# Optimization experiments

Hardware: AMD Instinct MI355X
Metric: run time of the kernel (lower is better)

The kernel has to match this reference:

```python
import jax, jax.numpy as jnp
import numpy as np
from jax import lax

N = 2048
B = 8
CH = 10
START = 1
STOP = 65


def setup_inputs() -> dict:
    key = jax.random.key(0)
    ks = jax.random.split(key, 13)

    def g(k, s):
        return jax.random.normal(k, s, jnp.float32) * 0.05

    return {
        "x": jax.random.normal(ks[0], (B, 1, N, N), jnp.float32),
        "wl": g(ks[1], (CH // 2, 1, 3, N)), "bl": g(ks[2], (CH // 2,)),
        "wr": g(ks[3], (CH // 2, 1, N, 3)), "br": g(ks[4], (CH // 2,)),
        "wA": g(ks[5], (CH, CH, 3)), "bA": g(ks[6], (CH,)),
        "wB": g(ks[7], (CH, CH, 3)), "bB": g(ks[8], (CH,)),  # shared by layers 2&3 (torch list aliasing)
        "wT": g(ks[9], (CH, CH, 3)), "bT": g(ks[10], (CH,)),
        "wm": g(ks[11], (2, CH, 1)), "bm": g(ks[12], (2,)),
        "start": START, "stop": STOP,
    }


def _conv1d(h, w, b, pad):
    y = lax.conv_general_dilated(h, w, (1,), [(pad, pad)], dimension_numbers=("NCH", "OIH", "NCH"))
    return y + b[None, :, None]


def _forward(x, wl, bl, wr, br, wA, bA, wB, bB, wT, bT, wm, bm, start, stop):
    n = x.shape[-1]
    # scan_left: Conv2d kernel (3, n), padding (1, 0) -> (B, 5, n, 1) -> squeeze
    left_ = lax.conv_general_dilated(x, wl, (1, 1), [(1, 1), (0, 0)], dimension_numbers=("NCHW", "OIHW", "NCHW"))
    left_ = left_[..., 0] + bl[None, :, None]
    # scan_right: Conv2d kernel (n, 3), padding (0, 1) -> (B, 5, 1, n) -> squeeze
    right_ = lax.conv_general_dilated(x, wr, (1, 1), [(0, 0), (1, 1)], dimension_numbers=("NCHW", "OIHW", "NCHW"))
    right_ = right_[:, :, 0, :] + br[None, :, None]
    lr = jnp.concatenate([left_, right_], axis=1)  # (B, 10, n)
    h = jax.nn.relu(_conv1d(lr, wA, bA, 1))
    h = jax.nn.relu(_conv1d(h, wB, bB, 1))  # same weights twice: torch [conv, relu]*2 aliasing
    h = jax.nn.relu(_conv1d(h, wB, bB, 1))
    # ConvTranspose1d(k=3, stride=1, pad=1) == Conv1d with transposed, spatially-flipped kernel, pad=1
    wTc = jnp.flip(jnp.swapaxes(wT, 0, 1), -1)
    for _ in range(3):
        h = jax.nn.relu(_conv1d(h, wTc, bT, 1))
    m = jax.nn.sigmoid(_conv1d(h, wm, bm, 0))  # (B, 2, n)
    left, right = m[:, 0, :], m[:, 1, :]
    xs = x[:, 0]  # (B, n, n)
    preds = []
    for d in range(start, stop):  # static diagonal indices
        curr = jnp.exp(jnp.diagonal(xs, offset=d, axis1=1, axis2=2))  # (B, n-d)
        mass_in = curr[:, 1:] * right[:, 1:n - d] + curr[:, :-1] * left[:, d:n - 1]
        mass_out = right[:, 0:n - d - 1] + left[:, d + 1:n]
        p = jnp.log(mass_in / mass_out)
        preds.append(p - jnp.mean(p))  # scalar mean over batch+positions, as torch.mean
    return jnp.concatenate(preds, axis=1)  # ragged preds concatenated: (B, sum(n-d-1))


def reference(x, wl, bl, wr, br, wA, bA, wB, bB, wT, bT, wm, bm, start, stop):
    return _forward(x, wl, bl, wr, br, wA, bA, wB, bB, wT, bT, wm, bm, start, stop)
```

## Files before the change

kernel.cpp:

```cpp
#include <hip/hip_runtime.h>
#include <hip/hip_bf16.h>

#define NN 2048
#define BB 8
#define TROW 128928

typedef __attribute__((ext_vector_type(8))) short bf16x8;
typedef __attribute__((ext_vector_type(4))) float f32x4;

__device__ __forceinline__ short f2bf(float f) {
    unsigned u = __float_as_uint(f);
    unsigned r = (u + 0x7FFFu + ((u >> 16) & 1u)) >> 16;
    return (short)r;
}

__global__ __launch_bounds__(256) void k_stage1(const float* __restrict__ x,
                                                const float* __restrict__ wl,
                                                const float* __restrict__ wr,
                                                float* __restrict__ Rp,
                                                float* __restrict__ CSp,
                                                float* __restrict__ psum,
                                                int* __restrict__ counter) {
    int blk = blockIdx.x;
    int tid = threadIdx.x;
    if (blk == 0 && tid < 65) {
        if (tid < 64) psum[tid] = 0.f;
        else *counter = 0;
    }
    if (blk < 1024) {
        int b = blk >> 7;
        int sub = blk & 127;
        int rg = sub >> 2, ks = sub & 3;
        int wv = tid >> 6, lane = tid & 63;
        int q = lane >> 4, m = lane & 15;
        int r0 = rg * 64 + wv * 16;
        int nrow = (m == 15) ? 14 : m;
        int k0 = ks * 512 + q * 8;

        const float* ap = x + ((size_t)(b * NN + r0 + m)) * NN + k0;
        const float* bp = wl + (size_t)nrow * NN + k0;

        f32x4 acc = {0.f, 0.f, 0.f, 0.f};
#pragma unroll 4
        for (int it = 0; it < 16; it++) {
            const float* a0 = ap + it * 32;
            const float* b0 = bp + it * 32;
            float4 av0 = *(const float4*)(a0);
            float4 av1 = *(const float4*)(a0 + 4);
            float4 bv0 = *(const float4*)(b0);
            float4 bv1 = *(const float4*)(b0 + 4);
            bf16x8 af, bf;
            af[0] = f2bf(av0.x); af[1] = f2bf(av0.y); af[2] = f2bf(av0.z); af[3] = f2bf(av0.w);
            af[4] = f2bf(av1.x); af[5] = f2bf(av1.y); af[6] = f2bf(av1.z); af[7] = f2bf(av1.w);
            bf[0] = f2bf(bv0.x); bf[1] = f2bf(bv0.y); bf[2] = f2bf(bv0.z); bf[3] = f2bf(bv0.w);
            bf[4] = f2bf(bv1.x); bf[5] = f2bf(bv1.y); bf[6] = f2bf(bv1.z); bf[7] = f2bf(bv1.w);
            acc = __builtin_amdgcn_mfma_f32_16x16x32_bf16(af, bf, acc, 0, 0, 0);
        }
        float* rp = Rp + (size_t)ks * 262144 + ((size_t)b * NN + r0) * 16;
#pragma unroll
        for (int reg = 0; reg < 4; reg++)
            rp[(q * 4 + reg) * 16 + m] = acc[reg];
    } else {
        int blk2 = blk - 1024;
        int b = blk2 >> 5;
        int rem = blk2 & 31;
        int jc = rem >> 4, rc = rem & 15;
        int r0 = rc * 128;
        int c0 = jc * 1024 + tid * 4;
        const float* xp = x + ((size_t)b * NN + r0) * NN + c0;

        float acc[15][4];
#pragma unroll
        for (int k = 0; k < 15; k++)
#pragma unroll
            for (int e = 0; e < 4; e++) acc[k][e] = 0.f;

        for (int rb = 0; rb < 16; rb++) {
            float4 xv[8];
#pragma unroll
            for (int q = 0; q < 8; q++)
                xv[q] = *(const float4*)(xp + (size_t)(rb * 8 + q) * NN);
#pragma unroll
            for (int q = 0; q < 8; q++) {
                int h = r0 + rb * 8 + q;
#pragma unroll
                for (int k = 0; k < 15; k++) {
                    int c = k / 3, dw = k - c * 3;
                    float wk = wr[c * (NN * 3) + h * 3 + dw];
                    acc[k][0] = fmaf(xv[q].x, wk, acc[k][0]);
                    acc[k][1] = fmaf(xv[q].y, wk, acc[k][1]);
                    acc[k][2] = fmaf(xv[q].z, wk, acc[k][2]);
                    acc[k][3] = fmaf(xv[q].w, wk, acc[k][3]);
                }
            }
        }
        float* outp = CSp + ((size_t)(rc * BB + b) * 16) * NN + c0;
#pragma unroll
        for (int k = 0; k < 15; k++) {
            float4 v; v.x = acc[k][0]; v.y = acc[k][1]; v.z = acc[k][2]; v.w = acc[k][3];
            *(float4*)(outp + (size_t)k * NN) = v;
        }
    }
}

__global__ __launch_bounds__(256) void k_csum(const float* __restrict__ CSp,
                                              float* __restrict__ CS,
                                              const float* __restrict__ Rp,
                                              float* __restrict__ R) {
    int blk = blockIdx.x;
    if (blk < 256) {
        int vid = blk * 256 + threadIdx.x;
        const float4* src = (const float4*)CSp;
        float4 s = src[vid];
#pragma unroll
        for (int rc = 1; rc < 16; rc++) {
            float4 v = src[vid + rc * 65536];
            s.x += v.x; s.y += v.y; s.z += v.z; s.w += v.w;
        }
        ((float4*)CS)[vid] = s;
    } else {
        int vid = (blk - 256) * 256 + threadIdx.x;
        const float4* src = (const float4*)Rp;
        float4 s = src[vid];
#pragma unroll
        for (int ks = 1; ks < 4; ks++) {
            float4 v = src[vid + ks * 65536];
            s.x += v.x; s.y += v.y; s.z += v.z; s.w += v.w;
        }
        ((float4*)R)[vid] = s;
    }
}

__global__ __launch_bounds__(256) void k_chainC(const float* __restrict__ R,
                                                const float* __restrict__ CS,
                                                const float* __restrict__ bl,
                                                const float* __restrict__ br,
                                                const float* __restrict__ wA, const float* __restrict__ bA,
                                                const float* __restrict__ wB, const float* __restrict__ bB,
                                                const float* __restrict__ wT, const float* __restrict__ bT,
                                                const float* __restrict__ wm, const float* __restrict__ bm,
                                                float* __restrict__ LEFT, float* __restrict__ RIGHT) {
    __shared__ float buf0[10][144], buf1[10][144];
    __shared__ float W[3][10][10][3];
    __shared__ float Bs[3][10];
    __shared__ float Wm[2][10], Bm[2];
    int b = blockIdx.x >> 4;
    int c0 = (blockIdx.x & 15) << 7;
    int tid = threadIdx.x;

    for (int idx = tid; idx < 900; idx += 256) {
        int set = idx / 300, rem = idx - set * 300;
        int o = rem / 30, rem2 = rem - o * 30, c = rem2 / 3, kk = rem2 - c * 3;
        float u;
        if (set == 0) u = wA[o * 30 + c * 3 + kk];
        else if (set == 1) u = wB[o * 30 + c * 3 + kk];
        else u = wT[c * 30 + o * 3 + (2 - kk)];
        W[set][o][c][kk] = u;
    }
    if (tid < 30) {
        float v = (tid < 10) ? bA[tid] : (tid < 20) ? bB[tid - 10] : bT[tid - 20];
        Bs[tid / 10][tid % 10] = v;
    }
    if (tid < 20) Wm[tid / 10][tid % 10] = wm[tid];
    if (tid < 2) Bm[tid] = bm[tid];

    for (int idx = tid; idx < 1400; idx += 256) {
        int ch = idx / 140, p = idx - ch * 140;
        int g = c0 - 6 + p;
        float v = 0.f;
        if (g >= 0 && g < NN) {
            if (ch < 5) {
                v = bl[ch];
#pragma unroll
                for (int dh = 0; dh < 3; dh++) {
                    int r = g + dh - 1;
                    if (r >= 0 && r < NN) v += R[(size_t)(b * NN + r) * 16 + ch * 3 + dh];
                }
            } else {
                int c = ch - 5;
                v = br[c];
#pragma unroll
                for (int dw = 0; dw < 3; dw++) {
                    int j = g + dw - 1;
                    if (j >= 0 && j < NN)
                        v += CS[((size_t)b * 16 + c * 3 + dw) * NN + j];
                }
            }
        }
        buf0[ch][p] = v;
    }
    __syncthreads();

    float(*in)[144] = buf0;
    float(*out)[144] = buf1;
    for (int layer = 0; layer < 6; layer++) {
        int set = (layer == 0) ? 0 : (layer < 3 ? 1 : 2);
        int lo = layer + 1;
        for (int idx = tid; idx < 1400; idx += 256) {
            int o = idx / 140, p = idx - o * 140;
            if (p >= lo && p < 140 - lo) {
                float s = Bs[set][o];
#pragma unroll
                for (int c = 0; c < 10; c++) {
                    const float* ip = &in[c][p];
                    s = fmaf(ip[-1], W[set][o][c][0], s);
                    s = fmaf(ip[0], W[set][o][c][1], s);
                    s = fmaf(ip[1], W[set][o][c][2], s);
                }
                s = s > 0.f ? s : 0.f;
                int g = c0 - 6 + p;
                if (g < 0 || g >= NN) s = 0.f;
                out[o][p] = s;
            }
        }
        __syncthreads();
        float(*tmp)[144] = in; in = out; out = tmp;
    }
    {
        int idx = tid;
        int o = idx >> 7, pp = idx & 127;
        int p = 6 + pp;
        float s = Bm[o];
#pragma unroll
        for (int c = 0; c < 10; c++) s = fmaf(in[c][p], Wm[o][c], s);
        float sig = 1.f / (1.f + __expf(-s));
        (o ? RIGHT : LEFT)[b * NN + c0 + pp] = sig;
    }
}

__global__ __launch_bounds__(256) void k_diagout(const float* __restrict__ x,
                                                 const float* __restrict__ LEFT,
                                                 const float* __restrict__ RIGHT,
                                                 float* __restrict__ psum,
                                                 int* __restrict__ counter,
                                                 float* __restrict__ outp) {
    __shared__ float T[65][65];
    __shared__ float psl[64];
    int b = blockIdx.x >> 5;
    int i0 = (blockIdx.x & 31) << 6;
    int tid = threadIdx.x;

    for (int idx = tid; idx < 65 * 64; idx += 256) {
        int r = idx >> 6, dm1 = idx & 63;
        int row = i0 + r;
        int col = row + dm1 + 1;
        float v = 0.f;
        if (row < NN && col < NN) v = __expf(x[((size_t)b * NN + row) * NN + col]);
        T[r][dm1] = v;
    }
    __syncthreads();

    int wv = tid >> 6, lane = tid & 63;
    int i = i0 + lane;
    const float* lf = LEFT + b * NN;
    const float* rt = RIGHT + b * NN;
    float pv[16];
#pragma unroll
    for (int s = 0; s < 16; s++) {
        int dm1 = wv * 16 + s;
        int d = dm1 + 1;
        int L = (NN - 1) - d;
        float p = 0.f;
        if (i < L) {
            float mi = T[lane + 1][dm1] * rt[i + 1] + T[lane][dm1] * lf[d + i];
            float mo = rt[i] + lf[d + 1 + i];
            p = __logf(mi / mo);
        }
        pv[s] = p;
        float s64 = p;
        for (int off = 32; off; off >>= 1) s64 += __shfl_down(s64, off);
        if (lane == 0) psl[dm1] = s64;
    }
    __syncthreads();
    if (tid < 64) atomicAdd(&psum[tid], psl[tid]);
    __syncthreads();
    if (tid == 0) {
        __threadfence();
        atomicAdd(counter, 1);
        while (__hip_atomic_load(counter, __ATOMIC_ACQUIRE, __HIP_MEMORY_SCOPE_AGENT) < 256) {}
    }
    __syncthreads();
    if (tid < 64)
        psl[tid] = __hip_atomic_load(&psum[tid], __ATOMIC_RELAXED, __HIP_MEMORY_SCOPE_AGENT);
    __syncthreads();

#pragma unroll
    for (int s = 0; s < 16; s++) {
        int dm1 = wv * 16 + s;
        int d = dm1 + 1;
        int L = (NN - 1) - d;
        if (i < L) {
            float mean = psl[dm1] / (float)(8 * L);
            size_t off0 = (size_t)dm1 * (NN - 1) - (size_t)dm1 * (dm1 + 1) / 2;
            outp[(size_t)b * TROW + off0 + i] = pv[s] - mean;
        }
    }
}

extern "C" void kernel_launch(void* const* d_in, const int* in_sizes, int n_in,
                              void* d_out, int out_size, void* d_ws, size_t ws_size,
                              hipStream_t stream) {
    const float* x = (const float*)d_in[0];
    const float* wl = (const float*)d_in[1];
    const float* bl = (const float*)d_in[2];
    const float* wr = (const float*)d_in[3];
    const float* br = (const float*)d_in[4];
    const float* wA = (const float*)d_in[5];
    const float* bA = (const float*)d_in[6];
    const float* wB = (const float*)d_in[7];
    const float* bB = (const float*)d_in[8];
    const float* wT = (const float*)d_in[9];
    const float* bT = (const float*)d_in[10];
    const float* wm = (const float*)d_in[11];
    const float* bm = (const float*)d_in[12];

    float* ws = (float*)d_ws;
    float* R    = ws;
    float* Rp   = ws + 262144;
    float* CSp  = ws + 1310720;
    float* CS   = ws + 5505024;
    float* LEFT = ws + 5767168;
    float* RIGHT= ws + 5783552;
    float* psum = ws + 5799936;
    int*   counter = (int*)(ws + 5800000);

    k_stage1<<<1280, 256, 0, stream>>>(x, wl, wr, Rp, CSp, psum, counter);
    k_csum<<<512, 256, 0, stream>>>(CSp, CS, Rp, R);
    k_chainC<<<128, 256, 0, stream>>>(R, CS, bl, br, wA, bA, wB, bB, wT, bT, wm, bm, LEFT, RIGHT);
    k_diagout<<<256, 256, 0, stream>>>(x, LEFT, RIGHT, psum, counter, (float*)d_out);
}
```

Baseline: 294.6 us.

## Fuse reduction, conv chain and diagonal output into one kernel with grid barrier

Removes the split-K partial sums for the left scan, so each block runs the full K=2048 reduction and writes R directly. It drops the separate csum kernel by folding the 16-way column-partial reduction into the conv-chain stage. The conv chain and diagonal-output kernels are merged into one 256-block kernel that uses a software grid barrier to exchange LEFT/RIGHT, cutting two launches and some workspace traffic. The costs are fewer blocks in the MFMA stage (less parallelism, longer serial K loop), redundant halo recomputation per 64-wide tile, and a spin barrier that assumes all 256 blocks are co-resident.

```diff
diff --git a/kernel.cpp b/kernel.cpp
--- a/kernel.cpp
+++ b/kernel.cpp
@@ -1,5 +1,4 @@
 #include <hip/hip_runtime.h>
-#include <hip/hip_bf16.h>
 
 #define NN 2048
 #define BB 8
@@ -17,32 +16,30 @@
 __global__ __launch_bounds__(256) void k_stage1(const float* __restrict__ x,
                                                 const float* __restrict__ wl,
                                                 const float* __restrict__ wr,
-                                                float* __restrict__ Rp,
+                                                float* __restrict__ R,
                                                 float* __restrict__ CSp,
                                                 float* __restrict__ psum,
-                                                int* __restrict__ counter) {
+                                                int* __restrict__ counters) {
     int blk = blockIdx.x;
     int tid = threadIdx.x;
-    if (blk == 0 && tid < 65) {
+    if (blk == 0) {
         if (tid < 64) psum[tid] = 0.f;
-        else *counter = 0;
-    }
-    if (blk < 1024) {
-        int b = blk >> 7;
-        int sub = blk & 127;
-        int rg = sub >> 2, ks = sub & 3;
+        else if (tid < 66) counters[tid - 64] = 0;
+    }
+    if (blk < 256) {
+        int b = blk >> 5;
+        int rg = blk & 31;
         int wv = tid >> 6, lane = tid & 63;
         int q = lane >> 4, m = lane & 15;
         int r0 = rg * 64 + wv * 16;
         int nrow = (m == 15) ? 14 : m;
-        int k0 = ks * 512 + q * 8;
-
-        const float* ap = x + ((size_t)(b * NN + r0 + m)) * NN + k0;
-        const float* bp = wl + (size_t)nrow * NN + k0;
+
+        const float* ap = x + ((size_t)(b * NN + r0 + m)) * NN + q * 8;
+        const float* bp = wl + (size_t)nrow * NN + q * 8;
 
         f32x4 acc = {0.f, 0.f, 0.f, 0.f};
 #pragma unroll 4
-        for (int it = 0; it < 16; it++) {
+        for (int it = 0; it < 64; it++) {
             const float* a0 = ap + it * 32;
             const float* b0 = bp + it * 32;
             float4 av0 = *(const float4*)(a0);
@@ -56,12 +53,12 @@
             bf[4] = f2bf(bv1.x); bf[5] = f2bf(bv1.y); bf[6] = f2bf(bv1.z); bf[7] = f2bf(bv1.w);
             acc = __builtin_amdgcn_mfma_f32_16x16x32_bf16(af, bf, acc, 0, 0, 0);
         }
-        float* rp = Rp + (size_t)ks * 262144 + ((size_t)b * NN + r0) * 16;
+        float* rp = R + ((size_t)b * NN + r0) * 16;
 #pragma unroll
         for (int reg = 0; reg < 4; reg++)
             rp[(q * 4 + reg) * 16 + m] = acc[reg];
     } else {
-        int blk2 = blk - 1024;
+        int blk2 = blk - 256;
         int b = blk2 >> 5;
         int rem = blk2 & 31;
         int jc = rem >> 4, rc = rem & 15;
@@ -103,50 +100,41 @@
     }
 }
 
-__global__ __launch_bounds__(256) void k_csum(const float* __restrict__ CSp,
-                                              float* __restrict__ CS,
-                                              const float* __restrict__ Rp,
-                                              float* __restrict__ R) {
-    int blk = blockIdx.x;
-    if (blk < 256) {
-        int vid = blk * 256 + threadIdx.x;
-        const float4* src = (const float4*)CSp;
-        float4 s = src[vid];
-#pragma unroll
-        for (int rc = 1; rc < 16; rc++) {
-            float4 v = src[vid + rc * 65536];
-            s.x += v.x; s.y += v.y; s.z += v.z; s.w += v.w;
-        }
-        ((float4*)CS)[vid] = s;
-    } else {
-        int vid = (blk - 256) * 256 + threadIdx.x;
-        const float4* src = (const float4*)Rp;
-        float4 s = src[vid];
-#pragma unroll
-        for (int ks = 1; ks < 4; ks++) {
-            float4 v = src[vid + ks * 65536];
-            s.x += v.x; s.y += v.y; s.z += v.z; s.w += v.w;
-        }
-        ((float4*)R)[vid] = s;
-    }
-}
-
-__global__ __launch_bounds__(256) void k_chainC(const float* __restrict__ R,
-                                                const float* __restrict__ CS,
-                                                const float* __restrict__ bl,
-                                                const float* __restrict__ br,
-                                                const float* __restrict__ wA, const float* __restrict__ bA,
-                                                const float* __restrict__ wB, const float* __restrict__ bB,
-                                                const float* __restrict__ wT, const float* __restrict__ bT,
-                                                const float* __restrict__ wm, const float* __restrict__ bm,
-                                                float* __restrict__ LEFT, float* __restrict__ RIGHT) {
-    __shared__ float buf0[10][144], buf1[10][144];
+__global__ __launch_bounds__(256) void k_rest(const float* __restrict__ x,
+                                              const float* __restrict__ R,
+                                              const float* __restrict__ CSp,
+                                              const float* __restrict__ bl,
+                                              const float* __restrict__ br,
+                                              const float* __restrict__ wA, const float* __restrict__ bA,
+                                              const float* __restrict__ wB, const float* __restrict__ bB,
+                                              const float* __restrict__ wT, const float* __restrict__ bT,
+                                              const float* __restrict__ wm, const float* __restrict__ bm,
+                                              float* __restrict__ LEFT, float* __restrict__ RIGHT,
+                                              float* __restrict__ psum,
+                                              int* __restrict__ counters,
+                                              float* __restrict__ outp) {
+    __shared__ float T[65][65];
+    __shared__ float buf0[10][80], buf1[10][80];
     __shared__ float W[3][10][10][3];
     __shared__ float Bs[3][10];
     __shared__ float Wm[2][10], Bm[2];
-    int b = blockIdx.x >> 4;
-    int c0 = (blockIdx.x & 15) << 7;
+    __shared__ float psl[64];
+    __shared__ float lfs[132], rts[68];
+
+    int b = blockIdx.x >> 5;
+    int t5 = blockIdx.x & 31;
+    int c0 = t5 << 6;
+    int i0 = t5 << 6;
     int tid = threadIdx.x;
+
+    for (int idx = tid; idx < 65 * 64; idx += 256) {
+        int r = idx >> 6, dm1 = idx & 63;
+        int row = i0 + r;
+        int col = row + dm1 + 1;
+        float v = 0.f;
+        if (row < NN && col < NN) v = __expf(x[((size_t)b * NN + row) * NN + col]);
+        T[r][dm1] = v;
+    }
 
     for (int idx = tid; idx < 900; idx += 256) {
         int set = idx / 300, rem = idx - set * 300;
@@ -164,8 +152,8 @@
     if (tid < 20) Wm[tid / 10][tid % 10] = wm[tid];
     if (tid < 2) Bm[tid] = bm[tid];
 
-    for (int idx = tid; idx < 1400; idx += 256) {
-        int ch = idx / 140, p = idx - ch * 140;
+    for (int idx = tid; idx < 760; idx += 256) {
+        int ch = idx / 76, p = idx - ch * 76;
         int g = c0 - 6 + p;
         float v = 0.f;
         if (g >= 0 && g < NN) {
@@ -182,8 +170,12 @@
 #pragma unroll
                 for (int dw = 0; dw < 3; dw++) {
                     int j = g + dw - 1;
-                    if (j >= 0 && j < NN)
-                        v += CS[((size_t)b * 16 + c * 3 + dw) * NN + j];
+                    if (j >= 0 && j < NN) {
+                        const float* csp = CSp + ((size_t)(b * 16) + c * 3 + dw) * NN + j;
+#pragma unroll
+                        for (int rc = 0; rc < 16; rc++)
+                            v += csp[(size_t)rc * (8 * 16 * NN)];
+                    }
                 }
             }
         }
@@ -191,14 +183,14 @@
     }
     __syncthreads();
 
-    float(*in)[144] = buf0;
-    float(*out)[144] = buf1;
+    float(*in)[80] = buf0;
+    float(*out)[80] = buf1;
     for (int layer = 0; layer < 6; layer++) {
         int set = (layer == 0) ? 0 : (layer < 3 ? 1 : 2);
         int lo = layer + 1;
-        for (int idx = tid; idx < 1400; idx += 256) {
-            int o = idx / 140, p = idx - o * 140;
-            if (p >= lo && p < 140 - lo) {
+        for (int idx = tid; idx < 760; idx += 256) {
+            int o = idx / 76, p = idx - o * 76;
+            if (p >= lo && p < 76 - lo) {
                 float s = Bs[set][o];
 #pragma unroll
                 for (int c = 0; c < 10; c++) {
@@ -214,46 +206,43 @@
             }
         }
         __syncthreads();
-        float(*tmp)[144] = in; in = out; out = tmp;
-    }
-    {
-        int idx = tid;
-        int o = idx >> 7, pp = idx & 127;
+        float(*tmp)[80] = in; in = out; out = tmp;
+    }
+    if (tid < 128) {
+        int o = tid >> 6, pp = tid & 63;
         int p = 6 + pp;
         float s = Bm[o];
 #pragma unroll
         for (int c = 0; c < 10; c++) s = fmaf(in[c][p], Wm[o][c], s);
         float sig = 1.f / (1.f + __expf(-s));
-        (o ? RIGHT : LEFT)[b * NN + c0 + pp] = sig;
-    }
-}
-
-__global__ __launch_bounds__(256) void k_diagout(const float* __restrict__ x,
-                                                 const float* __restrict__ LEFT,
-                                                 const float* __restrict__ RIGHT,
-                                                 float* __restrict__ psum,
-                                                 int* __restrict__ counter,
-                                                 float* __restrict__ outp) {
-    __shared__ float T[65][65];
-    __shared__ float psl[64];
-    int b = blockIdx.x >> 5;
-    int i0 = (blockIdx.x & 31) << 6;
-    int tid = threadIdx.x;
-
-    for (int idx = tid; idx < 65 * 64; idx += 256) {
-        int r = idx >> 6, dm1 = idx & 63;
-        int row = i0 + r;
-        int col = row + dm1 + 1;
-        float v = 0.f;
-        if (row < NN && col < NN) v = __expf(x[((size_t)b * NN + row) * NN + col]);
-        T[r][dm1] = v;
+        float* dst = (o ? RIGHT : LEFT) + b * NN + c0 + pp;
+        __hip_atomic_store(dst, sig, __ATOMIC_RELAXED, __HIP_MEMORY_SCOPE_AGENT);
+    }
+    __syncthreads();
+
+    if (tid == 0) {
+        __threadfence();
+        atomicAdd(&counters[0], 1);
+        while (__hip_atomic_load(&counters[0], __ATOMIC_ACQUIRE, __HIP_MEMORY_SCOPE_AGENT) < 256) {
+            __builtin_amdgcn_s_sleep(2);
+        }
+    }
+    __syncthreads();
+
+    if (tid < 195) {
+        if (tid < 129) {
+            int g = i0 + 1 + tid; if (g > NN - 1) g = NN - 1;
+            lfs[tid] = __hip_atomic_load(LEFT + b * NN + g, __ATOMIC_RELAXED, __HIP_MEMORY_SCOPE_AGENT);
+        } else {
+            int p2 = tid - 129;
+            int g = i0 + p2; if (g > NN - 1) g = NN - 1;
+            rts[p2] = __hip_atomic_load(RIGHT + b * NN + g, __ATOMIC_RELAXED, __HIP_MEMORY_SCOPE_AGENT);
+        }
     }
     __syncthreads();
 
     int wv = tid >> 6, lane = tid & 63;
     int i = i0 + lane;
-    const float* lf = LEFT + b * NN;
-    const float* rt = RIGHT + b * NN;
     float pv[16];
 #pragma unroll
     for (int s = 0; s < 16; s++) {
@@ -262,8 +251,8 @@
         int L = (NN - 1) - d;
         float p = 0.f;
         if (i < L) {
-            float mi = T[lane + 1][dm1] * rt[i + 1] + T[lane][dm1] * lf[d + i];
-            float mo = rt[i] + lf[d + 1 + i];
+            float mi = T[lane + 1][dm1] * rts[lane + 1] + T[lane][dm1] * lfs[dm1 + lane];
+            float mo = rts[lane] + lfs[dm1 + lane + 1];
             p = __logf(mi / mo);
         }
         pv[s] = p;
@@ -274,10 +263,13 @@
     __syncthreads();
     if (tid < 64) atomicAdd(&psum[tid], psl[tid]);
     __syncthreads();
+
     if (tid == 0) {
         __threadfence();
-        atomicAdd(counter, 1);
-        while (__hip_atomic_load(counter, __ATOMIC_ACQUIRE, __HIP_MEMORY_SCOPE_AGENT) < 256) {}
+        atomicAdd(&counters[1], 1);
+        while (__hip_atomic_load(&counters[1], __ATOMIC_ACQUIRE, __HIP_MEMORY_SCOPE_AGENT) < 256) {
+            __builtin_amdgcn_s_sleep(2);
+        }
     }
     __syncthreads();
     if (tid < 64)
@@ -315,17 +307,14 @@
     const float* bm = (const float*)d_in[12];
 
     float* ws = (float*)d_ws;
-    float* R    = ws;
-    float* Rp   = ws + 262144;
-    float* CSp  = ws + 1310720;
-    float* CS   = ws + 5505024;
-    float* LEFT = ws + 5767168;
-    float* RIGHT= ws + 5783552;
-    float* psum = ws + 5799936;
-    int*   counter = (int*)(ws + 5800000);
-
-    k_stage1<<<1280, 256, 0, stream>>>(x, wl, wr, Rp, CSp, psum, counter);
-    k_csum<<<512, 256, 0, stream>>>(CSp, CS, Rp, R);
-    k_chainC<<<128, 256, 0, stream>>>(R, CS, bl, br, wA, bA, wB, bB, wT, bT, wm, bm, LEFT, RIGHT);
-    k_diagout<<<256, 256, 0, stream>>>(x, LEFT, RIGHT, psum, counter, (float*)d_out);
+    float* R     = ws;
+    float* CSp   = ws + 262144;
+    float* LEFT  = ws + 4456448;
+    float* RIGHT = ws + 4472832;
+    float* psum  = ws + 4489216;
+    int*   counters = (int*)(ws + 4489280);
+
+    k_stage1<<<512, 256, 0, stream>>>(x, wl, wr, R, CSp, psum, counters);
+    k_rest<<<256, 256, 0, stream>>>(x, R, CSp, bl, br, wA, bA, wB, bB, wT, bT, wm, bm,
+                                    LEFT, RIGHT, psum, counters, (float*)d_out);
 }
```

New measurement: 288.8 us. 2.0% less time.
